# Kernel tuning notes

Measured on AMD Instinct MI355X. Metric: run time of the kernel, lower is better.

The kernel has to match this reference:

```python
import jax, jax.numpy as jnp
import numpy as np

N, B, H, L, FE = 32768, 256, 128, 4, 4
E = 262144


def setup_inputs() -> dict:
    key = jax.random.key(0)
    ks = jax.random.split(key, 16)
    def g(i, shape, scale=0.05):
        return jax.random.normal(ks[i], shape, dtype=jnp.float32) * scale
    return {
        "d": jax.random.uniform(ks[0], (E,), dtype=jnp.float32) * 5.0,
        "src": jax.random.randint(ks[1], (E,), 0, N),
        "dst": jax.random.randint(ks[2], (E,), 0, N),
        "seg": jnp.sort(jax.random.randint(ks[3], (N,), 0, B)),
        "node_emb": g(4, (H,), 1.0),
        "We": g(5, (2 * FE + 1, H)), "be": jnp.zeros((H,), jnp.float32),
        "msg_W1": g(6, (L, 3 * H, H)), "msg_b1": jnp.zeros((L, H), jnp.float32),
        "msg_W2": g(7, (L, H, H)), "msg_b2": jnp.zeros((L, H), jnp.float32),
        "soft_W": g(8, (L, H)), "soft_b": jnp.zeros((L,), jnp.float32),
        "upd_W1": g(9, (L, H, H)), "upd_b1": jnp.zeros((L, H), jnp.float32),
        "upd_W2": g(10, (L, H, H)), "upd_b2": jnp.zeros((L, H), jnp.float32),
        "out_W1": g(11, (H, H)), "out_b1": jnp.zeros((H,), jnp.float32),
        "out_W2": g(12, (H, H)), "out_b2": jnp.zeros((H,), jnp.float32),
    }


def reference(d, src, dst, seg, node_emb, We, be, msg_W1, msg_b1, msg_W2, msg_b2,
              soft_W, soft_b, upd_W1, upd_b1, upd_W2, upd_b2,
              out_W1, out_b1, out_W2, out_b2):
    silu = jax.nn.silu
    # fourier_encode_dist: [E] -> [E, 2*FE+1] = [sin(d/2^k), cos(d/2^k), d]
    scales = 2.0 ** jnp.arange(FE, dtype=d.dtype)
    x = d[:, None] / scales
    de = jnp.concatenate([jnp.sin(x), jnp.cos(x), d[:, None]], axis=-1)
    # edge_input MLP (1 layer, last_activation=SiLU) then extra F.silu in input_edge_func
    e = silu(silu(de @ We + be))                              # [E, H]
    # node_embedding broadcast to all nodes
    feat = jnp.broadcast_to(node_emb, (N, H))
    for l in range(L):
        mi = jnp.concatenate([feat[src], feat[dst], e], axis=-1)        # [E, 3H]
        m = silu(silu(mi @ msg_W1[l] + msg_b1[l]) @ msg_W2[l] + msg_b2[l])  # [E, H]
        e = e + m                                             # edge residual update
        w = jax.nn.sigmoid(m @ soft_W[l] + soft_b[l])[:, None]  # soft edge gate [E,1]
        msum = jax.ops.segment_sum(m * w, dst, num_segments=N)  # reduce to dst nodes
        upd_in = msum + feat
        feat = silu(upd_in @ upd_W1[l] + upd_b1[l]) @ upd_W2[l] + upd_b2[l] + feat
    # node-wise output network (2 layers, last activation None)
    feat = silu(feat @ out_W1 + out_b1) @ out_W2 + out_b2
    # multi-aggregator readout over graphs in batch
    s = jax.ops.segment_sum(feat, seg, num_segments=B)
    cnt = jax.ops.segment_sum(jnp.ones((N, 1), feat.dtype), seg, num_segments=B)
    mean = s / jnp.maximum(cnt, 1.0)
    mx = jax.ops.segment_max(feat, seg, num_segments=B)
    return jnp.concatenate([s, mean, mx], axis=-1)            # [B, 3H]
```

## Files before the change

kernel.cpp:

```cpp
#include <hip/hip_runtime.h>
#include <hip/hip_bf16.h>

#define NN 32768
#define NB 256
#define HD 128
#define NL 4
#define NE 262144

typedef short bf16x8 __attribute__((ext_vector_type(8)));
typedef float f32x4 __attribute__((ext_vector_type(4)));
typedef unsigned short u16;
typedef unsigned int u32;

__device__ __forceinline__ float bf2f(u16 u) {
  return __uint_as_float(((u32)u) << 16);
}
__device__ __forceinline__ u16 f2bf(float f) {
  u32 x = __float_as_uint(f);
  u32 r = x + 0x7FFFu + ((x >> 16) & 1u);
  return (u16)(r >> 16);
}
__device__ __forceinline__ u32 pk2(float a, float b) {
  __hip_bfloat162 h = __float22bfloat162_rn(make_float2(a, b));
  return *reinterpret_cast<u32*>(&h);
}
__device__ __forceinline__ float siluf(float x) {
  return x * __builtin_amdgcn_rcpf(1.0f + __expf(-x));
}
__device__ __forceinline__ float sigf(float x) {
  return __builtin_amdgcn_rcpf(1.0f + __expf(-x));
}
__device__ __forceinline__ u32 ordu(float f) {
  u32 b = __float_as_uint(f);
  return (b & 0x80000000u) ? ~b : (b | 0x80000000u);
}

__device__ __forceinline__ float ldinf(const void* p, size_t i, int mode) {
  return mode ? ((const float*)p)[i] : bf2f(((const u16*)p)[i]);
}
__device__ __forceinline__ u16 ldinb(const void* p, size_t i, int mode) {
  return mode ? f2bf(((const float*)p)[i]) : ((const u16*)p)[i];
}

__global__ void k_detect(const u16* __restrict__ Weraw, int* __restrict__ flag) {
  if (threadIdx.x == 0 && blockIdx.x == 0) {
    int cnt = 0;
    for (int i = 0; i < 256; i++) {
      u16 u = Weraw[2 * i];
      u32 e = (u >> 7) & 0xFFu;
      if (e >= 112u && e <= 126u) cnt++;
    }
    *flag = (cnt >= 128) ? 0 : 1;
  }
}


__global__ __launch_bounds__(256) void k_csr_deg(const int* __restrict__ dstp,
                                                 u32* __restrict__ deg) {
  const int i = blockIdx.x * 256 + threadIdx.x;
  atomicAdd(&deg[dstp[i]], 1u);
}

__global__ __launch_bounds__(1024) void k_csr_scan(const u32* __restrict__ deg,
                                                   int* __restrict__ rowptr,
                                                   int* __restrict__ cursor) {
  __shared__ int part[1024];
  const int t = threadIdx.x;
  int loc[32];
  int s = 0;
#pragma unroll
  for (int j = 0; j < 32; j++) { loc[j] = s; s += (int)deg[t * 32 + j]; }
  part[t] = s;
  __syncthreads();
  int inc = s;
  for (int off = 1; off < 1024; off <<= 1) {
    int tmp = (t >= off) ? part[t - off] : 0;
    __syncthreads();
    part[t] += tmp;
    __syncthreads();
  }
  const int base = part[t] - inc;
#pragma unroll
  for (int j = 0; j < 32; j++) {
    rowptr[t * 32 + j] = base + loc[j];
    cursor[t * 32 + j] = base + loc[j];
  }
  if (t == 1023) rowptr[NN] = part[1023];
}

__global__ __launch_bounds__(256) void k_csr_scatter(const int* __restrict__ dstp,
                                                     const int* __restrict__ srcp,
                                                     int* __restrict__ cursor,
                                                     int* __restrict__ eids,
                                                     int* __restrict__ src_s,
                                                     int* __restrict__ dst_s) {
  const int i = blockIdx.x * 256 + threadIdx.x;
  const int d = dstp[i];
  const int pos = atomicAdd(&cursor[d], 1);
  eids[pos] = i;
  src_s[pos] = srcp[i];
  dst_s[pos] = d;
}

#define PANEL 16384

template <int MT>
__device__ __forceinline__ void acc_zero(f32x4 (&acc)[MT][8]) {
#pragma unroll
  for (int mt = 0; mt < MT; mt++)
#pragma unroll
    for (int nt = 0; nt < 8; nt++) acc[mt][nt] = f32x4{0.f, 0.f, 0.f, 0.f};
}

__device__ __forceinline__ void load_a2(const u16* __restrict__ A0,
                                        const size_t* rowoff, int kg,
                                        bf16x8 (&a)[2][4]) {
#pragma unroll
  for (int ks = 0; ks < 4; ks++)
#pragma unroll
    for (int mt = 0; mt < 2; mt++)
      a[mt][ks] = *(const bf16x8*)&A0[rowoff[mt] + ks * 32 + kg * 8];
}

__device__ __forceinline__ void gemm_lds2(const bf16x8 (&a)[2][4],
                                          const short* sB, int l,
                                          f32x4 (&acc)[2][8]) {
#pragma unroll
  for (int ks = 0; ks < 4; ks++)
#pragma unroll
    for (int nt = 0; nt < 8; nt++) {
      bf16x8 b = *(const bf16x8*)&sB[((nt * 4 + ks) * 64 + l) * 8];
#pragma unroll
      for (int mt = 0; mt < 2; mt++)
        acc[mt][nt] = __builtin_amdgcn_mfma_f32_16x16x32_bf16(a[mt][ks], b, acc[mt][nt], 0, 0, 0);
    }
}

template <int MT>
__device__ __forceinline__ void wave_gemm_p(const short* lAw, const u16* __restrict__ Bp,
                                            int l, int c, int kg, f32x4 (&acc)[MT][8]) {
#pragma unroll
  for (int ks = 0; ks < 4; ks++) {
    bf16x8 a[MT];
#pragma unroll
    for (int mt = 0; mt < MT; mt++) {
      const int r = mt * 16 + c;
      const int k = ks * 32 + kg * 8;
      a[mt] = *(const bf16x8*)&lAw[r * HD + (k ^ ((r & 7) << 3))];
    }
#pragma unroll
    for (int nt = 0; nt < 8; nt++) {
      bf16x8 b = *(const bf16x8*)&Bp[(size_t)((nt * 4 + ks) * 64 + l) * 8];
#pragma unroll
      for (int mt = 0; mt < MT; mt++)
        acc[mt][nt] = __builtin_amdgcn_mfma_f32_16x16x32_bf16(a[mt], b, acc[mt][nt], 0, 0, 0);
    }
  }
}

template <int MT, bool SILU>
__device__ __forceinline__ void wave_pack(short* lAw, int c, int kg,
                                          f32x4 (&acc)[MT][8], const float* bias) {
#pragma unroll
  for (int mt = 0; mt < MT; mt++) {
#pragma unroll
    for (int rr = 0; rr < 4; rr++) {
      const int row = mt * 16 + kg * 4 + rr;
      u32 ou[4];
#pragma unroll
      for (int p = 0; p < 4; p++) {
        float x0 = acc[mt][2 * p][rr] + bias[2 * p];
        float x1 = acc[mt][2 * p + 1][rr] + bias[2 * p + 1];
        if (SILU) { x0 = siluf(x0); x1 = siluf(x1); }
        ou[p] = pk2(x0, x1);
      }
      ((int4*)(lAw + row * HD))[c ^ (row & 7)] =
          make_int4((int)ou[0], (int)ou[1], (int)ou[2], (int)ou[3]);
    }
  }
}

__device__ __forceinline__ void stage_panel(const u16* __restrict__ P,
                                            short* sB, int tid) {
#pragma unroll
  for (int it = 0; it < 8; it++) {
    const int idx = (it * 256 + tid) * 8;
    *(int4*)&sB[idx] = *(const int4*)&P[idx];
  }
}

__global__ __launch_bounds__(256) void k_prep(
    const void* __restrict__ mW1, const void* __restrict__ mW2,
    const void* __restrict__ uW1, const void* __restrict__ uW2,
    const void* __restrict__ oW1, const void* __restrict__ oW2,
    const int* __restrict__ flagp,
    u16* __restrict__ Wt1, u16* __restrict__ Wt2p,
    u16* __restrict__ Wtu1, u16* __restrict__ Wtu2p,
    u16* __restrict__ Wto1, u16* __restrict__ Wto2p) {
  const int mode = *flagp;
  const int tid = blockIdx.x * blockDim.x + threadIdx.x;
  const int stride = gridDim.x * blockDim.x;
  for (int i = tid; i < NL * 3 * PANEL; i += stride) {
    const int l = i / (3 * PANEL), r = i % (3 * PANEL);
    const int chunk = r / PANEL, r2 = r % PANEL;
    const int nt = r2 / 2048, ks = (r2 % 2048) / 512;
    const int lane = (r2 % 512) / 8, j = r2 % 8;
    const int s = ks * 32 + (lane >> 4) * 8 + j;
    const int klog = ((s & 7) << 4) | (s >> 3);
    const int n = nt * 16 + (lane & 15);
    Wt1[i] = ldinb(mW1, ((size_t)l * 384 + chunk * 128 + klog) * HD + n, mode);
  }
  for (int i = tid; i < NL * PANEL; i += stride) {
    const int l = i / PANEL, r = i % PANEL;
    const int nt = r / 2048, ks = (r % 2048) / 512;
    const int lane = (r % 512) / 8, j = r % 8;
    const int s = ks * 32 + (lane >> 4) * 8 + j;
    const int klog = ((s & 7) << 4) | (s >> 3);
    const int n = nt * 16 + (lane & 15);
    Wt2p[i] = ldinb(mW2, ((size_t)l * HD + klog) * HD + n, mode);
    Wtu1[i] = ldinb(uW1, ((size_t)l * HD + klog) * HD + n, mode);
    Wtu2p[i] = ldinb(uW2, ((size_t)l * HD + klog) * HD + n, mode);
  }
  for (int i = tid; i < PANEL; i += stride) {
    const int nt = i / 2048, ks = (i % 2048) / 512;
    const int lane = (i % 512) / 8, j = i % 8;
    const int s = ks * 32 + (lane >> 4) * 8 + j;
    const int klog = ((s & 7) << 4) | (s >> 3);
    const int n = nt * 16 + (lane & 15);
    Wto1[i] = ldinb(oW1, (size_t)klog * HD + n, mode);
    Wto2p[i] = ldinb(oW2, (size_t)klog * HD + n, mode);
  }
}

__global__ __launch_bounds__(256) void k_featinit(const void* __restrict__ nemb,
                                                  const int* __restrict__ flagp,
                                                  u16* __restrict__ feat) {
  const int mode = *flagp;
  const int i = blockIdx.x * 256 + threadIdx.x;
  const int g = i & 15;
  u32 ou[4];
#pragma unroll
  for (int p = 0; p < 4; p++) {
    u16 a = ldinb(nemb, (2 * p) * 16 + g, mode);
    u16 b = ldinb(nemb, (2 * p + 1) * 16 + g, mode);
    ou[p] = (u32)a | ((u32)b << 16);
  }
  ((int4*)feat)[i] = make_int4((int)ou[0], (int)ou[1], (int)ou[2], (int)ou[3]);
}

__global__ __launch_bounds__(256) void k_encode(const void* __restrict__ d,
                                                const int* __restrict__ eids,
                                                const void* __restrict__ We,
                                                const void* __restrict__ be,
                                                const int* __restrict__ flagp,
                                                u16* __restrict__ e) {
  const int mode = *flagp;
  __shared__ float sW[9 * HD];
  __shared__ float sb[HD];
  for (int i = threadIdx.x; i < 9 * HD; i += 256) sW[i] = ldinf(We, i, mode);
  for (int i = threadIdx.x; i < HD; i += 256) sb[i] = ldinf(be, i, mode);
  __syncthreads();
  const int spos = blockIdx.x * 256 + threadIdx.x;
  const float dv = ldinf(d, eids[spos], mode);
  float de[9];
#pragma unroll
  for (int k = 0; k < 4; k++) {
    float x = dv * (1.0f / (float)(1 << k));
    de[k] = __sinf(x);
    de[4 + k] = __cosf(x);
  }
  de[8] = dv;
  u16* erow = e + (size_t)spos * HD;
#pragma unroll
  for (int g = 0; g < 16; g++) {
    u32 ou[4];
#pragma unroll
    for (int p = 0; p < 4; p++) {
      float vv[2];
#pragma unroll
      for (int t = 0; t < 2; t++) {
        const int h = (2 * p + t) * 16 + g;
        float a = sb[h];
#pragma unroll
        for (int k = 0; k < 9; k++) a += de[k] * sW[k * HD + h];
        vv[t] = siluf(siluf(a));
      }
      ou[p] = pk2(vv[0], vv[1]);
    }
    ((int4*)erow)[g] = make_int4((int)ou[0], (int)ou[1], (int)ou[2], (int)ou[3]);
  }
}

__global__ __launch_bounds__(256, 2) void k_edge(
    const u16* __restrict__ feat, u16* __restrict__ e,
    const int* __restrict__ src_s, const int* __restrict__ dst_s,
    const u16* __restrict__ Wt1, const u16* __restrict__ Wt2p,
    const void* __restrict__ b1g, const void* __restrict__ b2g,
    const void* __restrict__ softW, const void* __restrict__ softb,
    const int* __restrict__ flagp, float* __restrict__ msum, int layer) {
  __shared__ __align__(16) short sB[PANEL];
  __shared__ __align__(16) short lM[128 * HD];
  __shared__ float swg[128];
  __shared__ int sdst[128];
  const int mode = *flagp;
  const int tid = threadIdx.x;
  const int l = tid & 63, wid = tid >> 6;
  const int c = l & 15, kg = l >> 4;
  const int bid = (int)blockIdx.x;
  const int blkB = (((bid & 7) << 8) | (bid >> 3)) * 128;
  const int blk = blkB + wid * 32;
  short* lMw = lM + wid * 32 * HD;
  float* swgw = swg + wid * 32;
  int* sdstw = sdst + wid * 32;

  if (l < 32) sdstw[l] = dst_s[blk + l];

  size_t offS[2], offD[2], offE[2];
#pragma unroll
  for (int mt = 0; mt < 2; mt++) {
    const int eidx = blk + mt * 16 + c;
    offS[mt] = (size_t)src_s[eidx] * HD;
    offD[mt] = (size_t)dst_s[eidx] * HD;
    offE[mt] = (size_t)eidx * HD;
  }

  const u16* W1l = Wt1 + (size_t)layer * 3 * PANEL;
  const u16* W2l = Wt2p + (size_t)layer * PANEL;
  float bias1[8], bias2[8], swf[8];
#pragma unroll
  for (int nt = 0; nt < 8; nt++) {
    bias1[nt] = ldinf(b1g, layer * HD + nt * 16 + c, mode);
    bias2[nt] = ldinf(b2g, layer * HD + nt * 16 + c, mode);
    swf[nt] = ldinf(softW, (size_t)layer * HD + nt * 16 + c, mode);
  }
  const float sbv = ldinf(softb, layer, mode);

  f32x4 acc[2][8];
  acc_zero<2>(acc);
  bf16x8 a[2][4];

  load_a2(feat, offS, kg, a);
  stage_panel(W1l, sB, tid);
  __syncthreads();
  gemm_lds2(a, sB, l, acc);
  __syncthreads();
  load_a2(feat, offD, kg, a);
  stage_panel(W1l + PANEL, sB, tid);
  __syncthreads();
  gemm_lds2(a, sB, l, acc);
  __syncthreads();
  load_a2(e, offE, kg, a);
  stage_panel(W1l + 2 * PANEL, sB, tid);
  __syncthreads();
  gemm_lds2(a, sB, l, acc);
  __syncthreads();

  stage_panel(W2l, sB, tid);
  wave_pack<2, true>(lMw, c, kg, acc, bias1);
  __syncthreads();

  acc_zero<2>(acc);
  wave_gemm_p<2>(lMw, (const u16*)sB, l, c, kg, acc);

  float wred[2][4];
#pragma unroll
  for (int mt = 0; mt < 2; mt++) {
#pragma unroll
    for (int rr = 0; rr < 4; rr++) {
      const int row = mt * 16 + kg * 4 + rr;
      int4* erow4 = (int4*)(e + (size_t)(blk + row) * HD);
      const int4 eo = erow4[c];
      const u32 eu[4] = {(u32)eo.x, (u32)eo.y, (u32)eo.z, (u32)eo.w};
      float mv[8];
      float wp = 0.f;
#pragma unroll
      for (int nt = 0; nt < 8; nt++) {
        mv[nt] = siluf(acc[mt][nt][rr] + bias2[nt]);
        wp += mv[nt] * swf[nt];
      }
      u32 mo[4], ou[4];
#pragma unroll
      for (int p = 0; p < 4; p++) {
        mo[p] = pk2(mv[2 * p], mv[2 * p + 1]);
        ou[p] = pk2(bf2f((u16)(eu[p] & 0xffffu)) + mv[2 * p],
                    bf2f((u16)(eu[p] >> 16)) + mv[2 * p + 1]);
      }
      ((int4*)(lMw + row * HD))[c ^ (row & 7)] =
          make_int4((int)mo[0], (int)mo[1], (int)mo[2], (int)mo[3]);
      erow4[c] = make_int4((int)ou[0], (int)ou[1], (int)ou[2], (int)ou[3]);
      wp += __shfl_xor(wp, 1);
      wp += __shfl_xor(wp, 2);
      wp += __shfl_xor(wp, 4);
      wp += __shfl_xor(wp, 8);
      wred[mt][rr] = wp;
    }
  }
#pragma unroll
  for (int mt = 0; mt < 2; mt++)
#pragma unroll
    for (int rr = 0; rr < 4; rr++)
      if (c == mt * 4 + rr) swgw[mt * 16 + kg * 4 + rr] = sigf(wred[mt][rr] + sbv);

  const int gM = ((l >> 3) << 3);
  const int em = l & 7;
  float a0 = 0.f, a1 = 0.f;
  int cur = sdstw[0];
  for (int r = 0; r < 32; r++) {
    const int dn = sdstw[r];
    if (dn != cur) {
      atomicAdd(&msum[(size_t)cur * HD + l], a0);
      atomicAdd(&msum[(size_t)cur * HD + l + 64], a1);
      a0 = 0.f; a1 = 0.f; cur = dn;
    }
    const int rx = (r & 7) << 3;
    const float wgr = swgw[r];
    a0 += wgr * bf2f((u16)lMw[r * HD + (gM ^ rx) + em]);
    a1 += wgr * bf2f((u16)lMw[r * HD + (gM ^ rx) + 64 + em]);
  }
  atomicAdd(&msum[(size_t)cur * HD + l], a0);
  atomicAdd(&msum[(size_t)cur * HD + l + 64], a1);
}

__global__ __launch_bounds__(64, 4) void k_node(
    u16* __restrict__ feat, float* __restrict__ msum,
    const u16* __restrict__ Wtu1, const u16* __restrict__ Wtu2p,
    const void* __restrict__ b1g, const void* __restrict__ b2g,
    const int* __restrict__ flagp, int layer) {
  __shared__ __align__(16) short lA[32 * HD];
  const int mode = *flagp;
  const int l = threadIdx.x;
  const int c = l & 15, kg = l >> 4;
  short* lAw = lA;
  const int bid = (int)blockIdx.x;
  const int blkn = (((bid & 7) << 7) | (bid >> 3)) * 32;
  const u16* W1l = Wtu1 + (size_t)layer * PANEL;
  const u16* W2l = Wtu2p + (size_t)layer * PANEL;
  float bias1[8], bias2[8];
#pragma unroll
  for (int nt = 0; nt < 8; nt++) {
    bias1[nt] = ldinf(b1g, layer * HD + nt * 16 + c, mode);
    bias2[nt] = ldinf(b2g, layer * HD + nt * 16 + c, mode);
  }
  const float4 z4 = make_float4(0.f, 0.f, 0.f, 0.f);
#pragma unroll
  for (int rp = 0; rp < 8; rp++) {
    const int r = rp * 4 + (l >> 4);
    const int g = l & 15;
    const int4 fv = ((const int4*)(feat + (size_t)(blkn + r) * HD))[g];
    const u32 uu[4] = {(u32)fv.x, (u32)fv.y, (u32)fv.z, (u32)fv.w};
    float4* mrow4 = (float4*)(msum + (size_t)(blkn + r) * HD);
    const float4 ma = mrow4[2 * g];
    const float4 mb = mrow4[2 * g + 1];
    mrow4[2 * g] = z4;
    mrow4[2 * g + 1] = z4;
    const float mm[8] = {ma.x, ma.y, ma.z, ma.w, mb.x, mb.y, mb.z, mb.w};
    u32 ou[4];
#pragma unroll
    for (int p = 0; p < 4; p++) {
      ou[p] = pk2(bf2f((u16)(uu[p] & 0xffffu)) + mm[2 * p],
                  bf2f((u16)(uu[p] >> 16)) + mm[2 * p + 1]);
    }
    ((int4*)(lAw + r * HD))[g ^ (r & 7)] =
        make_int4((int)ou[0], (int)ou[1], (int)ou[2], (int)ou[3]);
  }
  __syncthreads();
  f32x4 acc[2][8];
  acc_zero<2>(acc);
  wave_gemm_p<2>(lAw, W1l, l, c, kg, acc);
  __syncthreads();
  wave_pack<2, true>(lAw, c, kg, acc, bias1);
  __syncthreads();
  acc_zero<2>(acc);
  wave_gemm_p<2>(lAw, W2l, l, c, kg, acc);

#pragma unroll
  for (int mt = 0; mt < 2; mt++) {
#pragma unroll
    for (int rr = 0; rr < 4; rr++) {
      const int row = mt * 16 + kg * 4 + rr;
      int4* frow4 = (int4*)(feat + (size_t)(blkn + row) * HD);
      const int4 fo = frow4[c];
      const u32 fu[4] = {(u32)fo.x, (u32)fo.y, (u32)fo.z, (u32)fo.w};
      u32 ou[4];
#pragma unroll
      for (int p = 0; p < 4; p++) {
        const float x0 = acc[mt][2 * p][rr] + bias2[2 * p];
        const float x1 = acc[mt][2 * p + 1][rr] + bias2[2 * p + 1];
        ou[p] = pk2(bf2f((u16)(fu[p] & 0xffffu)) + x0,
                    bf2f((u16)(fu[p] >> 16)) + x1);
      }
      frow4[c] = make_int4((int)ou[0], (int)ou[1], (int)ou[2], (int)ou[3]);
    }
  }
}

__global__ __launch_bounds__(64, 4) void k_out(
    const u16* __restrict__ feat, const int* __restrict__ seg,
    const u16* __restrict__ Wto1, const u16* __restrict__ Wto2p,
    const void* __restrict__ ob1, const void* __restrict__ ob2,
    const int* __restrict__ flagp,
    float* __restrict__ sacc, u32* __restrict__ mxacc, float* __restrict__ cnt) {
  __shared__ __align__(16) short lA[32 * HD];
  __shared__ int sseg[32];
  const int mode = *flagp;
  const int l = threadIdx.x;
  const int c = l & 15, kg = l >> 4;
  short* lAw = lA;
  const int bid = (int)blockIdx.x;
  const int blkn = (((bid & 7) << 7) | (bid >> 3)) * 32;
  float bias1[8], bias2[8];
#pragma unroll
  for (int nt = 0; nt < 8; nt++) {
    bias1[nt] = ldinf(ob1, nt * 16 + c, mode);
    bias2[nt] = ldinf(ob2, nt * 16 + c, mode);
  }
#pragma unroll
  for (int rp = 0; rp < 8; rp++) {
    const int r = rp * 4 + (l >> 4);
    const int g = l & 15;
    ((int4*)(lAw + r * HD))[g ^ (r & 7)] =
        ((const int4*)(feat + (size_t)(blkn + r) * HD))[g];
  }
  if (l < 32) sseg[l] = seg[blkn + l];
  __syncthreads();
  f32x4 acc[2][8];
  acc_zero<2>(acc);
  wave_gemm_p<2>(lAw, Wto1, l, c, kg, acc);
  __syncthreads();
  wave_pack<2, true>(lAw, c, kg, acc, bias1);
  __syncthreads();
  acc_zero<2>(acc);
  wave_gemm_p<2>(lAw, Wto2p, l, c, kg, acc);
  __syncthreads();
  wave_pack<2, false>(lAw, c, kg, acc, bias2);
  __syncthreads();

  const int gL = l >> 2;
  const int eoff = (l & 3) * 2;
  const bool uniform = (sseg[0] == sseg[31]);
  if (uniform) {
    const int g = sseg[0];
    float s1 = 0.f, s2 = 0.f, x1 = -3.402823e38f, x2 = -3.402823e38f;
#pragma unroll 4
    for (int r = 0; r < 32; r++) {
      const u32 mv = *(const u32*)&lAw[r * HD + ((gL ^ (r & 7)) << 3) + eoff];
      const float v1 = bf2f((u16)(mv & 0xffffu));
      const float v2 = bf2f((u16)(mv >> 16));
      s1 += v1; s2 += v2;
      x1 = fmaxf(x1, v1); x2 = fmaxf(x2, v2);
    }
    atomicAdd(&sacc[(size_t)g * HD + 2 * l], s1);
    atomicAdd(&sacc[(size_t)g * HD + 2 * l + 1], s2);
    atomicMax(&mxacc[(size_t)g * HD + 2 * l], ordu(x1));
    atomicMax(&mxacc[(size_t)g * HD + 2 * l + 1], ordu(x2));
    if (l == 0) atomicAdd(&cnt[g], 32.0f);
  } else {
    if (l < 32) atomicAdd(&cnt[sseg[l]], 1.0f);
#pragma unroll 4
    for (int r = 0; r < 32; r++) {
      const u32 mv = *(const u32*)&lAw[r * HD + ((gL ^ (r & 7)) << 3) + eoff];
      const float v1 = bf2f((u16)(mv & 0xffffu));
      const float v2 = bf2f((u16)(mv >> 16));
      const int g = sseg[r];
      atomicAdd(&sacc[(size_t)g * HD + 2 * l], v1);
      atomicAdd(&sacc[(size_t)g * HD + 2 * l + 1], v2);
      atomicMax(&mxacc[(size_t)g * HD + 2 * l], ordu(v1));
      atomicMax(&mxacc[(size_t)g * HD + 2 * l + 1], ordu(v2));
    }
  }
}

__global__ __launch_bounds__(256) void k_final(const float* __restrict__ sacc,
                                               const u32* __restrict__ mxacc,
                                               const float* __restrict__ cnt,
                                               const int* __restrict__ flagp,
                                               void* __restrict__ out) {
  const int mode = *flagp;
  const int i = blockIdx.x * 256 + threadIdx.x;
  const int b = i / 384, j = i % 384;
  float v;
  if (j < HD) {
    const int p = ((j & 15) << 3) | (j >> 4);
    v = sacc[b * HD + p];
  } else if (j < 2 * HD) {
    const int t = j - HD;
    const int p = ((t & 15) << 3) | (t >> 4);
    v = sacc[b * HD + p] / fmaxf(cnt[b], 1.0f);
  } else {
    const int t = j - 2 * HD;
    const int p = ((t & 15) << 3) | (t >> 4);
    u32 u = mxacc[b * HD + p];
    u32 bits = (u >> 31) ? (u ^ 0x80000000u) : ~u;
    v = __uint_as_float(bits);
  }
  if (mode) ((float*)out)[i] = v;
  else ((u16*)out)[i] = f2bf(v);
}

extern "C" void kernel_launch(void* const* d_in, const int* in_sizes, int n_in,
                              void* d_out, int out_size, void* d_ws, size_t ws_size,
                              hipStream_t stream) {
  const void* d_d = d_in[0];
  const int* src = (const int*)d_in[1];
  const int* dst = (const int*)d_in[2];
  const int* seg = (const int*)d_in[3];
  const void* nemb = d_in[4];
  const void* We = d_in[5];
  const void* be = d_in[6];
  const void* mW1 = d_in[7];
  const void* mb1 = d_in[8];
  const void* mW2 = d_in[9];
  const void* mb2 = d_in[10];
  const void* sW = d_in[11];
  const void* sb = d_in[12];
  const void* uW1 = d_in[13];
  const void* ub1 = d_in[14];
  const void* uW2 = d_in[15];
  const void* ub2 = d_in[16];
  const void* oW1 = d_in[17];
  const void* ob1 = d_in[18];
  const void* oW2 = d_in[19];
  const void* ob2 = d_in[20];

  char* ws = (char*)d_ws;
  const size_t OFF_E = 0;
  const size_t OFF_MSUM = OFF_E + (size_t)NE * HD * 2;
  const size_t OFF_FEAT = OFF_MSUM + (size_t)NN * HD * 4;
  const size_t OFF_SACC = OFF_FEAT + (size_t)NN * HD * 2;
  const size_t OFF_MX = OFF_SACC + (size_t)NB * HD * 4;
  const size_t OFF_CNT = OFF_MX + (size_t)NB * HD * 4;
  const size_t OFF_DEG = OFF_CNT + 1024;
  const size_t OFF_ROWPTR = OFF_DEG + (size_t)NN * 4;
  const size_t OFF_CURSOR = OFF_ROWPTR + (size_t)(NN + 2) * 4;
  const size_t OFF_EIDS = OFF_CURSOR + (size_t)NN * 4;
  const size_t OFF_SRCS = OFF_EIDS + (size_t)NE * 4;
  const size_t OFF_DSTS = OFF_SRCS + (size_t)NE * 4;
  const size_t OFF_WT1 = OFF_DSTS + (size_t)NE * 4;
  const size_t OFF_WT2P = OFF_WT1 + (size_t)NL * 3 * PANEL * 2;
  const size_t OFF_WTU1 = OFF_WT2P + (size_t)NL * PANEL * 2;
  const size_t OFF_WTU2P = OFF_WTU1 + (size_t)NL * PANEL * 2;
  const size_t OFF_WTO1 = OFF_WTU2P + (size_t)NL * PANEL * 2;
  const size_t OFF_WTO2P = OFF_WTO1 + (size_t)PANEL * 2;
  const size_t OFF_FLAG = OFF_WTO2P + (size_t)PANEL * 2;

  u16* e = (u16*)(ws + OFF_E);
  float* msum = (float*)(ws + OFF_MSUM);
  u16* feat = (u16*)(ws + OFF_FEAT);
  float* sacc = (float*)(ws + OFF_SACC);
  u32* mx = (u32*)(ws + OFF_MX);
  float* cnt = (float*)(ws + OFF_CNT);
  u32* deg = (u32*)(ws + OFF_DEG);
  int* rowptr = (int*)(ws + OFF_ROWPTR);
  int* cursor = (int*)(ws + OFF_CURSOR);
  int* eids = (int*)(ws + OFF_EIDS);
  int* src_s = (int*)(ws + OFF_SRCS);
  int* dst_s = (int*)(ws + OFF_DSTS);
  u16* Wt1 = (u16*)(ws + OFF_WT1);
  u16* Wt2p = (u16*)(ws + OFF_WT2P);
  u16* Wtu1 = (u16*)(ws + OFF_WTU1);
  u16* Wtu2p = (u16*)(ws + OFF_WTU2P);
  u16* Wto1 = (u16*)(ws + OFF_WTO1);
  u16* Wto2p = (u16*)(ws + OFF_WTO2P);
  int* flag = (int*)(ws + OFF_FLAG);

  hipMemsetAsync(ws + OFF_SACC, 0,
                 (size_t)NB * HD * 4 * 2 + 1024 + (size_t)NN * 4, stream);
  hipMemsetAsync(msum, 0, (size_t)NN * HD * 4, stream);

  k_detect<<<1, 64, 0, stream>>>((const u16*)We, flag);
  k_prep<<<256, 256, 0, stream>>>(mW1, mW2, uW1, uW2, oW1, oW2, flag,
                                  Wt1, Wt2p, Wtu1, Wtu2p, Wto1, Wto2p);
  k_featinit<<<(NN * HD / 8) / 256, 256, 0, stream>>>(nemb, flag, feat);

  k_csr_deg<<<NE / 256, 256, 0, stream>>>(dst, deg);
  k_csr_scan<<<1, 1024, 0, stream>>>(deg, rowptr, cursor);
  k_csr_scatter<<<NE / 256, 256, 0, stream>>>(dst, src, cursor, eids, src_s, dst_s);

  k_encode<<<NE / 256, 256, 0, stream>>>(d_d, eids, We, be, flag, e);

  for (int l = 0; l < NL; l++) {
    k_edge<<<NE / 128, 256, 0, stream>>>(feat, e, src_s, dst_s, Wt1, Wt2p,
                                         mb1, mb2, sW, sb, flag, msum, l);
    k_node<<<NN / 32, 64, 0, stream>>>(feat, msum, Wtu1, Wtu2p, ub1, ub2, flag, l);
  }
  k_out<<<NN / 32, 64, 0, stream>>>(feat, seg, Wto1, Wto2p, ob1, ob2, flag, sacc, mx, cnt);
  k_final<<<(NB * 384) / 256, 256, 0, stream>>>(sacc, mx, cnt, flag, d_out);
}
```

Measured before the change: 741.5 us.

## Fold constant layer-0 node features into bias and fuse output MLP into last node kernel

At layer 0 every node feature equals node_emb, so the src and dst parts of the first message GEMM collapse to a constant vector. A tiny kernel precomputes that vector and adds it to bias1, which lets the layer-0 edge kernel skip two of its three K-panels and the feature gathers. The output MLP and readout are also fused into the last k_node launch, so feat is never written back and reread. The precomputed vector is in fp32 while the skipped path used bf16 GEMMs, so results may differ slightly.

```diff
diff --git a/kernel.cpp b/kernel.cpp
--- a/kernel.cpp
+++ b/kernel.cpp
@@ -54,6 +54,17 @@
   }
 }
 
+__global__ void k_v0(const void* __restrict__ nemb, const void* __restrict__ mW1,
+                     const int* __restrict__ flagp, float* __restrict__ v0f) {
+  const int mode = *flagp;
+  const int n = threadIdx.x;
+  float s = 0.f;
+  for (int k = 0; k < 256; k++)
+    s += ldinf(nemb, k & 127, mode) * ldinf(mW1, (size_t)k * HD + n, mode);
+  v0f[n] = s;
+}
+
+#define PANEL 16384
 
 __global__ __launch_bounds__(256) void k_csr_deg(const int* __restrict__ dstp,
                                                  u32* __restrict__ deg) {
@@ -101,8 +112,6 @@
   src_s[pos] = srcp[i];
   dst_s[pos] = d;
 }
-
-#define PANEL 16384
 
 template <int MT>
 __device__ __forceinline__ void acc_zero(f32x4 (&acc)[MT][8]) {
@@ -291,13 +300,15 @@
   }
 }
 
+template <bool FIRST>
 __global__ __launch_bounds__(256, 2) void k_edge(
     const u16* __restrict__ feat, u16* __restrict__ e,
     const int* __restrict__ src_s, const int* __restrict__ dst_s,
     const u16* __restrict__ Wt1, const u16* __restrict__ Wt2p,
     const void* __restrict__ b1g, const void* __restrict__ b2g,
     const void* __restrict__ softW, const void* __restrict__ softb,
-    const int* __restrict__ flagp, float* __restrict__ msum, int layer) {
+    const int* __restrict__ flagp, const float* __restrict__ v0f,
+    float* __restrict__ msum, int layer) {
   __shared__ __align__(16) short sB[PANEL];
   __shared__ __align__(16) short lM[128 * HD];
   __shared__ float swg[128];
@@ -319,8 +330,10 @@
 #pragma unroll
   for (int mt = 0; mt < 2; mt++) {
     const int eidx = blk + mt * 16 + c;
-    offS[mt] = (size_t)src_s[eidx] * HD;
-    offD[mt] = (size_t)dst_s[eidx] * HD;
+    if (!FIRST) {
+      offS[mt] = (size_t)src_s[eidx] * HD;
+      offD[mt] = (size_t)dst_s[eidx] * HD;
+    }
     offE[mt] = (size_t)eidx * HD;
   }
 
@@ -330,6 +343,7 @@
 #pragma unroll
   for (int nt = 0; nt < 8; nt++) {
     bias1[nt] = ldinf(b1g, layer * HD + nt * 16 + c, mode);
+    if (FIRST) bias1[nt] += v0f[nt * 16 + c];
     bias2[nt] = ldinf(b2g, layer * HD + nt * 16 + c, mode);
     swf[nt] = ldinf(softW, (size_t)layer * HD + nt * 16 + c, mode);
   }
@@ -339,16 +353,18 @@
   acc_zero<2>(acc);
   bf16x8 a[2][4];
 
-  load_a2(feat, offS, kg, a);
-  stage_panel(W1l, sB, tid);
-  __syncthreads();
-  gemm_lds2(a, sB, l, acc);
-  __syncthreads();
-  load_a2(feat, offD, kg, a);
-  stage_panel(W1l + PANEL, sB, tid);
-  __syncthreads();
-  gemm_lds2(a, sB, l, acc);
-  __syncthreads();
+  if (!FIRST) {
+    load_a2(feat, offS, kg, a);
+    stage_panel(W1l, sB, tid);
+    __syncthreads();
+    gemm_lds2(a, sB, l, acc);
+    __syncthreads();
+    load_a2(feat, offD, kg, a);
+    stage_panel(W1l + PANEL, sB, tid);
+    __syncthreads();
+    gemm_lds2(a, sB, l, acc);
+    __syncthreads();
+  }
   load_a2(e, offE, kg, a);
   stage_panel(W1l + 2 * PANEL, sB, tid);
   __syncthreads();
@@ -421,12 +437,18 @@
   atomicAdd(&msum[(size_t)cur * HD + l + 64], a1);
 }
 
+template <bool LAST>
 __global__ __launch_bounds__(64, 4) void k_node(
     u16* __restrict__ feat, float* __restrict__ msum,
     const u16* __restrict__ Wtu1, const u16* __restrict__ Wtu2p,
     const void* __restrict__ b1g, const void* __restrict__ b2g,
-    const int* __restrict__ flagp, int layer) {
+    const int* __restrict__ flagp, int layer,
+    const int* __restrict__ seg,
+    const u16* __restrict__ Wto1, const u16* __restrict__ Wto2p,
+    const void* __restrict__ ob1, const void* __restrict__ ob2,
+    float* __restrict__ sacc, u32* __restrict__ mxacc, float* __restrict__ cnt) {
   __shared__ __align__(16) short lA[32 * HD];
+  __shared__ int sseg[32];
   const int mode = *flagp;
   const int l = threadIdx.x;
   const int c = l & 15, kg = l >> 4;
@@ -441,6 +463,8 @@
     bias1[nt] = ldinf(b1g, layer * HD + nt * 16 + c, mode);
     bias2[nt] = ldinf(b2g, layer * HD + nt * 16 + c, mode);
   }
+  if (LAST && l < 32) sseg[l] = seg[blkn + l];
+
   const float4 z4 = make_float4(0.f, 0.f, 0.f, 0.f);
 #pragma unroll
   for (int rp = 0; rp < 8; rp++) {
@@ -472,6 +496,7 @@
   __syncthreads();
   acc_zero<2>(acc);
   wave_gemm_p<2>(lAw, W2l, l, c, kg, acc);
+  __syncthreads();
 
 #pragma unroll
   for (int mt = 0; mt < 2; mt++) {
@@ -489,83 +514,66 @@
         ou[p] = pk2(bf2f((u16)(fu[p] & 0xffffu)) + x0,
                     bf2f((u16)(fu[p] >> 16)) + x1);
       }
-      frow4[c] = make_int4((int)ou[0], (int)ou[1], (int)ou[2], (int)ou[3]);
-    }
-  }
-}
-
-__global__ __launch_bounds__(64, 4) void k_out(
-    const u16* __restrict__ feat, const int* __restrict__ seg,
-    const u16* __restrict__ Wto1, const u16* __restrict__ Wto2p,
-    const void* __restrict__ ob1, const void* __restrict__ ob2,
-    const int* __restrict__ flagp,
-    float* __restrict__ sacc, u32* __restrict__ mxacc, float* __restrict__ cnt) {
-  __shared__ __align__(16) short lA[32 * HD];
-  __shared__ int sseg[32];
-  const int mode = *flagp;
-  const int l = threadIdx.x;
-  const int c = l & 15, kg = l >> 4;
-  short* lAw = lA;
-  const int bid = (int)blockIdx.x;
-  const int blkn = (((bid & 7) << 7) | (bid >> 3)) * 32;
-  float bias1[8], bias2[8];
-#pragma unroll
-  for (int nt = 0; nt < 8; nt++) {
-    bias1[nt] = ldinf(ob1, nt * 16 + c, mode);
-    bias2[nt] = ldinf(ob2, nt * 16 + c, mode);
-  }
-#pragma unroll
-  for (int rp = 0; rp < 8; rp++) {
-    const int r = rp * 4 + (l >> 4);
-    const int g = l & 15;
-    ((int4*)(lAw + r * HD))[g ^ (r & 7)] =
-        ((const int4*)(feat + (size_t)(blkn + r) * HD))[g];
-  }
-  if (l < 32) sseg[l] = seg[blkn + l];
-  __syncthreads();
-  f32x4 acc[2][8];
-  acc_zero<2>(acc);
-  wave_gemm_p<2>(lAw, Wto1, l, c, kg, acc);
-  __syncthreads();
-  wave_pack<2, true>(lAw, c, kg, acc, bias1);
-  __syncthreads();
-  acc_zero<2>(acc);
-  wave_gemm_p<2>(lAw, Wto2p, l, c, kg, acc);
-  __syncthreads();
-  wave_pack<2, false>(lAw, c, kg, acc, bias2);
-  __syncthreads();
-
-  const int gL = l >> 2;
-  const int eoff = (l & 3) * 2;
-  const bool uniform = (sseg[0] == sseg[31]);
-  if (uniform) {
-    const int g = sseg[0];
-    float s1 = 0.f, s2 = 0.f, x1 = -3.402823e38f, x2 = -3.402823e38f;
+      const int4 nv = make_int4((int)ou[0], (int)ou[1], (int)ou[2], (int)ou[3]);
+      if (LAST) {
+        ((int4*)(lAw + row * HD))[c ^ (row & 7)] = nv;
+      } else {
+        frow4[c] = nv;
+      }
+    }
+  }
+
+  if (LAST) {
+    __syncthreads();
+    float ob1r[8], ob2r[8];
+#pragma unroll
+    for (int nt = 0; nt < 8; nt++) {
+      ob1r[nt] = ldinf(ob1, nt * 16 + c, mode);
+      ob2r[nt] = ldinf(ob2, nt * 16 + c, mode);
+    }
+    acc_zero<2>(acc);
+    wave_gemm_p<2>(lAw, Wto1, l, c, kg, acc);
+    __syncthreads();
+    wave_pack<2, true>(lAw, c, kg, acc, ob1r);
+    __syncthreads();
+    acc_zero<2>(acc);
+    wave_gemm_p<2>(lAw, Wto2p, l, c, kg, acc);
+    __syncthreads();
+    wave_pack<2, false>(lAw, c, kg, acc, ob2r);
+    __syncthreads();
+
+    const int gL = l >> 2;
+    const int eoff = (l & 3) * 2;
+    const bool uniform = (sseg[0] == sseg[31]);
+    if (uniform) {
+      const int g = sseg[0];
+      float s1 = 0.f, s2 = 0.f, x1 = -3.402823e38f, x2 = -3.402823e38f;
 #pragma unroll 4
-    for (int r = 0; r < 32; r++) {
-      const u32 mv = *(const u32*)&lAw[r * HD + ((gL ^ (r & 7)) << 3) + eoff];
-      const float v1 = bf2f((u16)(mv & 0xffffu));
-      const float v2 = bf2f((u16)(mv >> 16));
-      s1 += v1; s2 += v2;
-      x1 = fmaxf(x1, v1); x2 = fmaxf(x2, v2);
-    }
-    atomicAdd(&sacc[(size_t)g * HD + 2 * l], s1);
-    atomicAdd(&sacc[(size_t)g * HD + 2 * l + 1], s2);
-    atomicMax(&mxacc[(size_t)g * HD + 2 * l], ordu(x1));
-    atomicMax(&mxacc[(size_t)g * HD + 2 * l + 1], ordu(x2));
-    if (l == 0) atomicAdd(&cnt[g], 32.0f);
-  } else {
-    if (l < 32) atomicAdd(&cnt[sseg[l]], 1.0f);
+      for (int r = 0; r < 32; r++) {
+        const u32 mv = *(const u32*)&lAw[r * HD + ((gL ^ (r & 7)) << 3) + eoff];
+        const float v1 = bf2f((u16)(mv & 0xffffu));
+        const float v2 = bf2f((u16)(mv >> 16));
+        s1 += v1; s2 += v2;
+        x1 = fmaxf(x1, v1); x2 = fmaxf(x2, v2);
+      }
+      atomicAdd(&sacc[(size_t)g * HD + 2 * l], s1);
+      atomicAdd(&sacc[(size_t)g * HD + 2 * l + 1], s2);
+      atomicMax(&mxacc[(size_t)g * HD + 2 * l], ordu(x1));
+      atomicMax(&mxacc[(size_t)g * HD + 2 * l + 1], ordu(x2));
+      if (l == 0) atomicAdd(&cnt[g], 32.0f);
+    } else {
+      if (l < 32) atomicAdd(&cnt[sseg[l]], 1.0f);
 #pragma unroll 4
-    for (int r = 0; r < 32; r++) {
-      const u32 mv = *(const u32*)&lAw[r * HD + ((gL ^ (r & 7)) << 3) + eoff];
-      const float v1 = bf2f((u16)(mv & 0xffffu));
-      const float v2 = bf2f((u16)(mv >> 16));
-      const int g = sseg[r];
-      atomicAdd(&sacc[(size_t)g * HD + 2 * l], v1);
-      atomicAdd(&sacc[(size_t)g * HD + 2 * l + 1], v2);
-      atomicMax(&mxacc[(size_t)g * HD + 2 * l], ordu(v1));
-      atomicMax(&mxacc[(size_t)g * HD + 2 * l + 1], ordu(v2));
+      for (int r = 0; r < 32; r++) {
+        const u32 mv = *(const u32*)&lAw[r * HD + ((gL ^ (r & 7)) << 3) + eoff];
+        const float v1 = bf2f((u16)(mv & 0xffffu));
+        const float v2 = bf2f((u16)(mv >> 16));
+        const int g = sseg[r];
+        atomicAdd(&sacc[(size_t)g * HD + 2 * l], v1);
+        atomicAdd(&sacc[(size_t)g * HD + 2 * l + 1], v2);
+        atomicMax(&mxacc[(size_t)g * HD + 2 * l], ordu(v1));
+        atomicMax(&mxacc[(size_t)g * HD + 2 * l + 1], ordu(v2));
+      }
     }
   }
 }
@@ -642,6 +650,7 @@
   const size_t OFF_WTO1 = OFF_WTU2P + (size_t)NL * PANEL * 2;
   const size_t OFF_WTO2P = OFF_WTO1 + (size_t)PANEL * 2;
   const size_t OFF_FLAG = OFF_WTO2P + (size_t)PANEL * 2;
+  const size_t OFF_V0 = OFF_FLAG + 64;
 
   u16* e = (u16*)(ws + OFF_E);
   float* msum = (float*)(ws + OFF_MSUM);
@@ -662,12 +671,14 @@
   u16* Wto1 = (u16*)(ws + OFF_WTO1);
   u16* Wto2p = (u16*)(ws + OFF_WTO2P);
   int* flag = (int*)(ws + OFF_FLAG);
+  float* v0f = (float*)(ws + OFF_V0);
 
   hipMemsetAsync(ws + OFF_SACC, 0,
                  (size_t)NB * HD * 4 * 2 + 1024 + (size_t)NN * 4, stream);
   hipMemsetAsync(msum, 0, (size_t)NN * HD * 4, stream);
 
   k_detect<<<1, 64, 0, stream>>>((const u16*)We, flag);
+  k_v0<<<1, 128, 0, stream>>>(nemb, mW1, flag, v0f);
   k_prep<<<256, 256, 0, stream>>>(mW1, mW2, uW1, uW2, oW1, oW2, flag,
                                   Wt1, Wt2p, Wtu1, Wtu2p, Wto1, Wto2p);
   k_featinit<<<(NN * HD / 8) / 256, 256, 0, stream>>>(nemb, flag, feat);
@@ -679,10 +690,20 @@
   k_encode<<<NE / 256, 256, 0, stream>>>(d_d, eids, We, be, flag, e);
 
   for (int l = 0; l < NL; l++) {
-    k_edge<<<NE / 128, 256, 0, stream>>>(feat, e, src_s, dst_s, Wt1, Wt2p,
-                                         mb1, mb2, sW, sb, flag, msum, l);
-    k_node<<<NN / 32, 64, 0, stream>>>(feat, msum, Wtu1, Wtu2p, ub1, ub2, flag, l);
-  }
-  k_out<<<NN / 32, 64, 0, stream>>>(feat, seg, Wto1, Wto2p, ob1, ob2, flag, sacc, mx, cnt);
+    if (l == 0)
+      k_edge<true><<<NE / 128, 256, 0, stream>>>(feat, e, src_s, dst_s, Wt1, Wt2p,
+                                                 mb1, mb2, sW, sb, flag, v0f, msum, l);
+    else
+      k_edge<false><<<NE / 128, 256, 0, stream>>>(feat, e, src_s, dst_s, Wt1, Wt2p,
+                                                  mb1, mb2, sW, sb, flag, v0f, msum, l);
+    if (l < NL - 1)
+      k_node<false><<<NN / 32, 64, 0, stream>>>(feat, msum, Wtu1, Wtu2p, ub1, ub2,
+                                                flag, l, seg, Wto1, Wto2p, ob1, ob2,
+                                                sacc, mx, cnt);
+    else
+      k_node<true><<<NN / 32, 64, 0, stream>>>(feat, msum, Wtu1, Wtu2p, ub1, ub2,
+                                               flag, l, seg, Wto1, Wto2p, ob1, ob2,
+                                               sacc, mx, cnt);
+  }
   k_final<<<(NB * 384) / 256, 256, 0, stream>>>(sacc, mx, cnt, flag, d_out);
 }
```

Measured after the change: 717.9 us. 3.2% less time.
